# Optimization experiments

Measured on AMD Instinct MI355X. Metric: run time of the kernel, lower is better.

The kernel has to match this reference:

```python
import jax, jax.numpy as jnp
import numpy as np

K_HEADS, D_HEAD = 8, 8
D = K_HEADS * D_HEAD  # 64


def _fc(x, W, b=None, relu=False):
    # 1x1 Conv2D over (B,T,N,C) == per-position dense
    y = x @ W
    if b is not None:
        y = y + b
    return jax.nn.relu(y) if relu else y


def _split_heads(x):
    # (B,T,N,K*d) -> (K,B,T,N,d); matches torch.cat(torch.split(x, d, -1), 0)
    B, T, N, _ = x.shape
    return x.reshape(B, T, N, K_HEADS, D_HEAD).transpose(3, 0, 1, 2, 4)


def _merge_heads(x):
    # (K,B,T,N,d) -> (B,T,N,K*d); matches torch.cat(torch.split(x, B, 0), -1)
    K, B, T, N, d = x.shape
    return x.transpose(1, 2, 3, 0, 4).reshape(B, T, N, K * d)


def _forward(X, TLE, key_padding_mask, *P):
    (sa_Wq, sa_bq, sa_Wk, sa_bk, sa_Wv, sa_bv, sa_Wo1, sa_bo1, sa_Wo2, sa_bo2,
     ta_Wq, ta_bq, ta_Wk, ta_bk, ta_Wv, ta_bv, ta_Wo1, ta_bo1, ta_Wo2, ta_bo2,
     g_Wxs, g_Wxt, g_bxt, g_Wh1, g_bh1, g_Wh2, g_bh2) = P
    B, T, N, _ = X.shape
    scale = 1.0 / (D_HEAD ** 0.5)
    XE = jnp.concatenate([X, TLE], axis=-1)  # (B,T,N,3D)

    # ---- Spatial attention (over nodes) ----
    q = _split_heads(_fc(XE, sa_Wq, sa_bq, True))
    k = _split_heads(_fc(XE, sa_Wk, sa_bk, True))
    v = _split_heads(_fc(XE, sa_Wv, sa_bv, True))
    s = jnp.einsum('kbtnd,kbtmd->kbtnm', q, k) * scale  # (K,B,T,N,N)
    p = jax.nn.softmax(s, axis=-1)
    HS = _merge_heads(jnp.einsum('kbtnm,kbtmd->kbtnd', p, v))
    HS = _fc(_fc(HS, sa_Wo1, sa_bo1, True), sa_Wo2, sa_bo2)

    # ---- Temporal attention (over time, causal + key padding) ----
    q = _split_heads(_fc(XE, ta_Wq, ta_bq, True))
    k = _split_heads(_fc(XE, ta_Wk, ta_bk, True))
    v = _split_heads(_fc(XE, ta_Wv, ta_bv, True))
    s = jnp.einsum('kbind,kbjnd->kbnij', q, k) * scale  # (K,B,N,T,T)
    causal = jnp.tril(jnp.ones((T, T), dtype=bool))  # (T,T)
    valid_key = jnp.arange(T)[None, :] < key_padding_mask  # (B,T)
    m = causal[None, None, None] & valid_key[None, :, None, None, :]
    s = jnp.where(m, s, -jnp.inf)
    p = jax.nn.softmax(s, axis=-1)
    HT = _merge_heads(jnp.einsum('kbnij,kbjnd->kbind', p, v))
    HT = _fc(_fc(HT, ta_Wo1, ta_bo1, True), ta_Wo2, ta_bo2)

    # ---- Gated fusion + residual ----
    z = jax.nn.sigmoid(HS @ g_Wxs + HT @ g_Wxt + g_bxt)
    H = z * HS + (1.0 - z) * HT
    H = _fc(_fc(H, g_Wh1, g_bh1, True), g_Wh2, g_bh2)
    return X + H


_PARAM_SHAPES = []
for _pre in ('sa', 'ta'):
    _PARAM_SHAPES += [(_pre + '_Wq', (3 * D, D)), (_pre + '_bq', (D,)),
                      (_pre + '_Wk', (3 * D, D)), (_pre + '_bk', (D,)),
                      (_pre + '_Wv', (3 * D, D)), (_pre + '_bv', (D,)),
                      (_pre + '_Wo1', (D, D)), (_pre + '_bo1', (D,)),
                      (_pre + '_Wo2', (D, D)), (_pre + '_bo2', (D,))]
_PARAM_SHAPES += [('g_Wxs', (D, D)), ('g_Wxt', (D, D)), ('g_bxt', (D,)),
                  ('g_Wh1', (D, D)), ('g_bh1', (D,)),
                  ('g_Wh2', (D, D)), ('g_bh2', (D,))]


def setup_inputs() -> dict:
    key = jax.random.key(0)
    ks = jax.random.split(key, 3 + len(_PARAM_SHAPES))
    B, T, N = 16, 24, 128
    inp = {
        'X': jax.random.normal(ks[0], (B, T, N, D), dtype=jnp.float32),
        'TLE': jax.random.normal(ks[1], (B, T, N, 2 * D), dtype=jnp.float32),
        'key_padding_mask': jax.random.randint(ks[2], (B, 1), 1, T + 1),
    }
    for i, (nm, shp) in enumerate(_PARAM_SHAPES):
        inp[nm] = jax.random.normal(ks[3 + i], shp, dtype=jnp.float32) * 0.05
    return inp


def reference(X, TLE, key_padding_mask,
              sa_Wq, sa_bq, sa_Wk, sa_bk, sa_Wv, sa_bv, sa_Wo1, sa_bo1, sa_Wo2, sa_bo2,
              ta_Wq, ta_bq, ta_Wk, ta_bk, ta_Wv, ta_bv, ta_Wo1, ta_bo1, ta_Wo2, ta_bo2,
              g_Wxs, g_Wxt, g_bxt, g_Wh1, g_bh1, g_Wh2, g_bh2):
    return _forward(X, TLE, key_padding_mask,
                    sa_Wq, sa_bq, sa_Wk, sa_bk, sa_Wv, sa_bv, sa_Wo1, sa_bo1, sa_Wo2, sa_bo2,
                    ta_Wq, ta_bq, ta_Wk, ta_bk, ta_Wv, ta_bv, ta_Wo1, ta_bo1, ta_Wo2, ta_bo2,
                    g_Wxs, g_Wxt, g_bxt, g_Wh1, g_bh1, g_Wh2, g_bh2)
```

## Files before the change

kernel.cpp:

```cpp
#include <hip/hip_runtime.h>
#include <math.h>

#define BB 16
#define TT 24
#define NN 128
#define DD 64
#define PTOT (BB * TT * NN)
#define P64  (PTOT * 64)

typedef __attribute__((ext_vector_type(8))) short bf16x8;
typedef __attribute__((ext_vector_type(4))) float f32x4;
typedef __attribute__((ext_vector_type(16))) float f32x16;

__device__ __forceinline__ unsigned short f2bf(float f) {
    unsigned u = __builtin_bit_cast(unsigned, f);
    u = (u + 0x7fffu + ((u >> 16) & 1u)) >> 16;
    return (unsigned short)u;
}
__device__ __forceinline__ void unpack8(uint4 u, float* f) {
    f[0] = __builtin_bit_cast(float, u.x << 16);
    f[1] = __builtin_bit_cast(float, u.x & 0xFFFF0000u);
    f[2] = __builtin_bit_cast(float, u.y << 16);
    f[3] = __builtin_bit_cast(float, u.y & 0xFFFF0000u);
    f[4] = __builtin_bit_cast(float, u.z << 16);
    f[5] = __builtin_bit_cast(float, u.z & 0xFFFF0000u);
    f[6] = __builtin_bit_cast(float, u.w << 16);
    f[7] = __builtin_bit_cast(float, u.w & 0xFFFF0000u);
}
__device__ __forceinline__ uint4 pack8(const float* f) {
    uint4 o;
    o.x = (unsigned)f2bf(f[0]) | ((unsigned)f2bf(f[1]) << 16);
    o.y = (unsigned)f2bf(f[2]) | ((unsigned)f2bf(f[3]) << 16);
    o.z = (unsigned)f2bf(f[4]) | ((unsigned)f2bf(f[5]) << 16);
    o.w = (unsigned)f2bf(f[6]) | ((unsigned)f2bf(f[7]) << 16);
    return o;
}
__device__ __forceinline__ float fast_exp2(float x) {
#if __has_builtin(__builtin_amdgcn_exp2f)
    return __builtin_amdgcn_exp2f(x);
#else
    return exp2f(x);
#endif
}
__device__ __forceinline__ unsigned cvt_pk_bf16(float a, float b) {
    unsigned r;
    asm("v_cvt_pk_bf16_f32 %0, %1, %2" : "=v"(r) : "v"(a), "v"(b));
    return r;
}
__device__ __forceinline__ f32x16 zero16() {
    f32x16 z;
    #pragma unroll
    for (int i = 0; i < 16; ++i) z[i] = 0.f;
    return z;
}

__global__ __launch_bounds__(256) void wprep_all(
    const float* __restrict__ W0, const float* __restrict__ W1,
    const float* __restrict__ W2, const float* __restrict__ W3,
    const float* __restrict__ W4, const float* __restrict__ W5,
    const float* __restrict__ E0, const float* __restrict__ E1,
    const float* __restrict__ E2, const float* __restrict__ E3,
    const float* __restrict__ E4, const float* __restrict__ E5,
    const float* __restrict__ E6, const float* __restrict__ E7,
    unsigned short* __restrict__ Wt, unsigned short* __restrict__ Wt8)
{
    const int bid = blockIdx.x;
    if (bid < 288) {
        const float* Ws[6] = {W0, W1, W2, W3, W4, W5};
        const int e = bid * 256 + threadIdx.x;
        const int j = e / 12288;
        const int r = e % 12288;
        const int k = r / 64;
        const int n = r % 64;
        Wt[j * 12288 + n * 192 + k] = f2bf(Ws[j][k * 64 + n]);
    } else {
        const float* Es[8] = {E0, E1, E2, E3, E4, E5, E6, E7};
        const int e = (bid - 288) * 256 + threadIdx.x;
        const int mat = e >> 12;
        const int r = e & 4095;
        const int k = r >> 6;
        const int n = r & 63;
        Wt8[mat * 4096 + n * 64 + k] = f2bf(Es[mat][k * 64 + n]);
    }
}

__global__ __launch_bounds__(256, 2) void fused_sattn(
    const float* __restrict__ X, const float* __restrict__ TLE,
    const unsigned short* __restrict__ Wt,
    const float* __restrict__ b0, const float* __restrict__ b1,
    const float* __restrict__ b2, const float* __restrict__ b3,
    const float* __restrict__ b4, const float* __restrict__ b5,
    unsigned short* __restrict__ qt, unsigned short* __restrict__ kt,
    unsigned short* __restrict__ vt,
    unsigned short* __restrict__ HS)
{
    __shared__ __align__(16) unsigned short xe[2][16][200];
    __shared__ __align__(16) unsigned short qq[128 * 64];
    __shared__ __align__(16) unsigned short kk[128 * 64];
    __shared__ __align__(16) unsigned short vv[128 * 64];
    const int tid = threadIdx.x;
    const long p0 = (long)blockIdx.x * 128;
    const int w = tid >> 6, l = tid & 63, quad = l >> 4, l16 = l & 15;

    auto stage = [&](int mt, int buf) {
        #pragma unroll
        for (int i = 0; i < 3; ++i) {
            const int idx4 = tid + i * 256;
            const int m  = idx4 / 48;
            const int kq = idx4 % 48;
            const int k  = kq * 4;
            const long p = p0 + mt * 16 + m;
            float4 v;
            if (k < 64) v = *reinterpret_cast<const float4*>(X + p * 64 + k);
            else        v = *reinterpret_cast<const float4*>(TLE + p * 128 + (k - 64));
            ushort4 pk;
            pk.x = f2bf(v.x); pk.y = f2bf(v.y); pk.z = f2bf(v.z); pk.w = f2bf(v.w);
            *reinterpret_cast<ushort4*>(&xe[buf][m][k]) = pk;
        }
    };

    bf16x8 wf[6][6];
    #pragma unroll
    for (int mat = 0; mat < 6; ++mat)
        #pragma unroll
        for (int kc = 0; kc < 6; ++kc)
            wf[mat][kc] = *reinterpret_cast<const bf16x8*>(
                &Wt[mat * 12288 + (w * 16 + l16) * 192 + kc * 32 + quad * 8]);

    const float* bias_p[6] = {b0, b1, b2, b3, b4, b5};
    float4 bias[6];
    #pragma unroll
    for (int mat = 0; mat < 6; ++mat)
        bias[mat] = *reinterpret_cast<const float4*>(&bias_p[mat][w * 16 + quad * 4]);

    stage(0, 0);
    __syncthreads();

    const int chunkW = ((w * 2 + (quad >> 1)));
    const int chSub  = (quad & 1) * 4;
    const int chBase = w * 16 + quad * 4;
    const float cs = 0.35355339059327373f * 1.4426950408889634f;

    for (int mt = 0; mt < 8; ++mt) {
        if (mt < 7) stage(mt + 1, (mt + 1) & 1);

        bf16x8 A[6];
        #pragma unroll
        for (int kc = 0; kc < 6; ++kc)
            A[kc] = *reinterpret_cast<const bf16x8*>(
                &xe[mt & 1][l16][kc * 32 + quad * 8]);

        f32x4 acc[6];
        #pragma unroll
        for (int mat = 0; mat < 6; ++mat) acc[mat] = (f32x4){0.f, 0.f, 0.f, 0.f};
        #pragma unroll
        for (int kc = 0; kc < 6; ++kc)
            #pragma unroll
            for (int mat = 0; mat < 6; ++mat)
                acc[mat] = __builtin_amdgcn_mfma_f32_16x16x32_bf16(
                    wf[mat][kc], A[kc], acc[mat], 0, 0, 0);

        const int pos = mt * 16 + l16;
        const int sw  = pos * 64 + ((chunkW ^ (pos & 7)) << 3) + chSub;
        unsigned short* dstS[3] = {qq, kk, vv};
        #pragma unroll
        for (int mat = 0; mat < 3; ++mat) {
            const float sc = (mat == 0) ? cs : 1.0f;
            ushort4 pk;
            pk.x = f2bf(fmaxf(acc[mat][0] + bias[mat].x, 0.f) * sc);
            pk.y = f2bf(fmaxf(acc[mat][1] + bias[mat].y, 0.f) * sc);
            pk.z = f2bf(fmaxf(acc[mat][2] + bias[mat].z, 0.f) * sc);
            pk.w = f2bf(fmaxf(acc[mat][3] + bias[mat].w, 0.f) * sc);
            *reinterpret_cast<ushort4*>(&dstS[mat][sw]) = pk;
        }
        unsigned short* dstT[3] = {qt, kt, vt};
        const long gp = (p0 + pos) * 64 + chBase;
        #pragma unroll
        for (int m3 = 3; m3 < 6; ++m3) {
            ushort4 pk;
            pk.x = f2bf(fmaxf(acc[m3][0] + bias[m3].x, 0.f));
            pk.y = f2bf(fmaxf(acc[m3][1] + bias[m3].y, 0.f));
            pk.z = f2bf(fmaxf(acc[m3][2] + bias[m3].z, 0.f));
            pk.w = f2bf(fmaxf(acc[m3][3] + bias[m3].w, 0.f));
            *reinterpret_cast<ushort4*>(&dstT[m3 - 3][gp]) = pk;
        }
        if (mt < 7) {
            __builtin_amdgcn_sched_barrier(0);
            asm volatile("s_waitcnt lgkmcnt(0)" ::: "memory");
            __builtin_amdgcn_s_barrier();
            __builtin_amdgcn_sched_barrier(0);
        }
    }

    const int hi = l >> 5;
    const int ln = l & 31;
    bf16x8 zf = {};

    auto pvstep = [&](f32x16& st, const bf16x8& va0, const bf16x8& va1,
                      f32x16& oacc) {
        const unsigned P0 = cvt_pk_bf16(st[0],  st[1]);
        const unsigned P1 = cvt_pk_bf16(st[2],  st[3]);
        const unsigned P2 = cvt_pk_bf16(st[4],  st[5]);
        const unsigned P3 = cvt_pk_bf16(st[6],  st[7]);
        const unsigned P4 = cvt_pk_bf16(st[8],  st[9]);
        const unsigned P5 = cvt_pk_bf16(st[10], st[11]);
        const unsigned P6 = cvt_pk_bf16(st[12], st[13]);
        const unsigned P7 = cvt_pk_bf16(st[14], st[15]);
        const unsigned V0 = __shfl_xor(hi ? P0 : P2, 32);
        const unsigned V1 = __shfl_xor(hi ? P1 : P3, 32);
        const unsigned V2 = __shfl_xor(hi ? P4 : P6, 32);
        const unsigned V3 = __shfl_xor(hi ? P5 : P7, 32);
        uint4 fe, fo;
        fe.x = hi ? V0 : P0; fe.y = hi ? V1 : P1;
        fe.z = hi ? P2 : V0; fe.w = hi ? P3 : V1;
        fo.x = hi ? V2 : P4; fo.y = hi ? V3 : P5;
        fo.z = hi ? P6 : V2; fo.w = hi ? P7 : V3;
        oacc = __builtin_amdgcn_mfma_f32_32x32x16_bf16(
            va0, __builtin_bit_cast(bf16x8, fe), oacc, 0, 0, 0);
        oacc = __builtin_amdgcn_mfma_f32_32x32x16_bf16(
            va1, __builtin_bit_cast(bf16x8, fo), oacc, 0, 0, 0);
    };

    #pragma unroll
    for (int hh2 = 0; hh2 < 2; ++hh2) {
        const int h = w * 2 + hh2;
        const int swz = (h ^ (ln & 7)) << 3;

        bf16x8 kf0 = hi ? zf : *reinterpret_cast<const bf16x8*>(&kk[(0 * 32 + ln) * 64 + swz]);
        bf16x8 kf1 = hi ? zf : *reinterpret_cast<const bf16x8*>(&kk[(1 * 32 + ln) * 64 + swz]);
        bf16x8 kf2 = hi ? zf : *reinterpret_cast<const bf16x8*>(&kk[(2 * 32 + ln) * 64 + swz]);
        bf16x8 kf3 = hi ? zf : *reinterpret_cast<const bf16x8*>(&kk[(3 * 32 + ln) * 64 + swz]);

        bf16x8 vf[8];
        #pragma unroll
        for (int c = 0; c < 8; ++c) {
            bf16x8 f = zf;
            if (ln < 8) {
                #pragma unroll
                for (int j = 0; j < 8; ++j) {
                    const int m = c * 16 + hi * 8 + j;
                    f[j] = (short)vv[m * 64 + ((h ^ (m & 7)) << 3) + ln];
                }
            }
            vf[c] = f;
        }

        #pragma unroll
        for (int nt = 0; nt < 4; ++nt) {
            const int qrow = nt * 32 + ln;
            bf16x8 qf = hi ? zf : *reinterpret_cast<const bf16x8*>(&qq[qrow * 64 + swz]);

            f32x16 st0 = zero16(), st1 = zero16(), st2 = zero16(), st3 = zero16();
            st0 = __builtin_amdgcn_mfma_f32_32x32x16_bf16(kf0, qf, st0, 0, 0, 0);
            st1 = __builtin_amdgcn_mfma_f32_32x32x16_bf16(kf1, qf, st1, 0, 0, 0);
            st2 = __builtin_amdgcn_mfma_f32_32x32x16_bf16(kf2, qf, st2, 0, 0, 0);
            st3 = __builtin_amdgcn_mfma_f32_32x32x16_bf16(kf3, qf, st3, 0, 0, 0);

            float sum = 0.f;
            #pragma unroll
            for (int r = 0; r < 16; ++r) { st0[r] = fast_exp2(st0[r]); sum += st0[r]; }
            #pragma unroll
            for (int r = 0; r < 16; ++r) { st1[r] = fast_exp2(st1[r]); sum += st1[r]; }
            #pragma unroll
            for (int r = 0; r < 16; ++r) { st2[r] = fast_exp2(st2[r]); sum += st2[r]; }
            #pragma unroll
            for (int r = 0; r < 16; ++r) { st3[r] = fast_exp2(st3[r]); sum += st3[r]; }
            sum += __shfl_xor(sum, 32);

            f32x16 oacc = zero16();
            pvstep(st0, vf[0], vf[1], oacc);
            pvstep(st1, vf[2], vf[3], oacc);
            pvstep(st2, vf[4], vf[5], oacc);
            pvstep(st3, vf[6], vf[7], oacc);

            const float inv = 1.0f / sum;
            ushort4 pk;
            pk.x = f2bf(oacc[0] * inv);
            pk.y = f2bf(oacc[1] * inv);
            pk.z = f2bf(oacc[2] * inv);
            pk.w = f2bf(oacc[3] * inv);
            *reinterpret_cast<ushort4*>(&HS[(p0 + qrow) * 64 + h * 8 + hi * 4]) = pk;
        }
    }
}

__global__ __launch_bounds__(192) void tattn_kernel(
    const unsigned short* __restrict__ Q, const unsigned short* __restrict__ Kb,
    const unsigned short* __restrict__ V, const int* __restrict__ kpm,
    unsigned short* __restrict__ O)
{
    __shared__ float kk[8][TT][8];
    __shared__ float vv[8][TT][8];
    const int tid = threadIdx.x;
    const int n = blockIdx.x & (NN - 1);
    const int b = blockIdx.x >> 7;

    {
        const int hs = tid / TT;
        const int j  = tid % TT;
        const long g = (((long)(b * TT + j)) * NN + n) * 64 + hs * 8;
        uint4 ku = *reinterpret_cast<const uint4*>(&Kb[g]);
        uint4 vu = *reinterpret_cast<const uint4*>(&V[g]);
        float kf[8], vf[8];
        unpack8(ku, kf); unpack8(vu, vf);
        #pragma unroll
        for (int d = 0; d < 8; ++d) { kk[hs][j][d] = kf[d]; vv[hs][j][d] = vf[d]; }
    }

    const int h = tid / TT;
    const int i = tid % TT;
    const long qb = (((long)(b * TT + i)) * NN + n) * 64 + h * 8;
    float q[8];
    {
        uint4 qu = *reinterpret_cast<const uint4*>(&Q[qb]);
        unpack8(qu, q);
    }
    __syncthreads();

    const int kp = kpm[b];
    const float scale = 0.35355339059327373f;

    float s[TT];
    #pragma unroll
    for (int j = 0; j < TT; ++j) {
        float t = 0.0f;
        #pragma unroll
        for (int d = 0; d < 8; ++d) t = fmaf(q[d], kk[h][j][d], t);
        s[j] = (j <= i && j < kp) ? t * scale : -INFINITY;
    }
    float mx = -INFINITY;
    #pragma unroll
    for (int j = 0; j < TT; ++j) mx = fmaxf(mx, s[j]);

    float sum = 0.0f;
    float acc[8];
    #pragma unroll
    for (int d = 0; d < 8; ++d) acc[d] = 0.0f;
    #pragma unroll
    for (int j = 0; j < TT; ++j) {
        const float e = __expf(s[j] - mx);
        sum += e;
        #pragma unroll
        for (int d = 0; d < 8; ++d) acc[d] = fmaf(e, vv[h][j][d], acc[d]);
    }
    const float inv = 1.0f / sum;
    float o[8];
    #pragma unroll
    for (int d = 0; d < 8; ++d) o[d] = acc[d] * inv;
    *reinterpret_cast<uint4*>(&O[qb]) = pack8(o);
}

__global__ __launch_bounds__(256) void epi_kernel(
    const float* __restrict__ X,
    const unsigned short* __restrict__ HSb, const unsigned short* __restrict__ HTb,
    const unsigned short* __restrict__ Wt8,
    const float* __restrict__ sbo1, const float* __restrict__ sbo2,
    const float* __restrict__ tbo1, const float* __restrict__ tbo2,
    const float* __restrict__ bxt,
    const float* __restrict__ bh1, const float* __restrict__ bh2,
    float* __restrict__ out)
{
    constexpr int RS = 72;
    __shared__ __align__(16) unsigned short bufA[64][RS], bufB[64][RS], bufC[64][RS];
    const int tid = threadIdx.x;
    const long p0 = (long)blockIdx.x * 64;
    const int w = tid >> 6, l = tid & 63, quad = l >> 4, l16 = l & 15;
    const int chBase = w * 16 + quad * 4;

    #pragma unroll
    for (int i = 0; i < 4; ++i) {
        const int idx = tid + i * 256;
        const int m = idx >> 4;
        const int c = (idx & 15) * 4;
        *reinterpret_cast<ushort4*>(&bufA[m][c]) =
            *reinterpret_cast<const ushort4*>(&HSb[(p0 + m) * 64 + c]);
        *reinterpret_cast<ushort4*>(&bufC[m][c]) =
            *reinterpret_cast<const ushort4*>(&HTb[(p0 + m) * 64 + c]);
    }
    __syncthreads();

    auto gemm = [&](const unsigned short (*in)[RS], int mat,
                    const float* __restrict__ bias, f32x4* accO) {
        bf16x8 af[2];
        #pragma unroll
        for (int kc = 0; kc < 2; ++kc)
            af[kc] = *reinterpret_cast<const bf16x8*>(
                &Wt8[mat * 4096 + (w * 16 + l16) * 64 + kc * 32 + quad * 8]);
        const float4 b4 = *reinterpret_cast<const float4*>(&bias[chBase]);
        #pragma unroll
        for (int pt = 0; pt < 4; ++pt) {
            f32x4 acc = (f32x4){0.f, 0.f, 0.f, 0.f};
            #pragma unroll
            for (int kc = 0; kc < 2; ++kc) {
                bf16x8 bf = *reinterpret_cast<const bf16x8*>(
                    &in[pt * 16 + l16][kc * 32 + quad * 8]);
                acc = __builtin_amdgcn_mfma_f32_16x16x32_bf16(af[kc], bf, acc, 0, 0, 0);
            }
            acc[0] += b4.x; acc[1] += b4.y; acc[2] += b4.z; acc[3] += b4.w;
            accO[pt] = acc;
        }
    };

    auto writeBuf = [&](unsigned short (*dst)[RS], const f32x4* v, bool relu) {
        #pragma unroll
        for (int pt = 0; pt < 4; ++pt) {
            float a0 = v[pt][0], a1 = v[pt][1], a2 = v[pt][2], a3 = v[pt][3];
            if (relu) { a0 = fmaxf(a0, 0.f); a1 = fmaxf(a1, 0.f);
                        a2 = fmaxf(a2, 0.f); a3 = fmaxf(a3, 0.f); }
            ushort4 pk; pk.x = f2bf(a0); pk.y = f2bf(a1); pk.z = f2bf(a2); pk.w = f2bf(a3);
            *reinterpret_cast<ushort4*>(&dst[pt * 16 + l16][chBase]) = pk;
        }
    };

    f32x4 t[4], HSr[4], HTr[4];

    gemm(bufA, 0, sbo1, t);
    __syncthreads();
    writeBuf(bufB, t, true);
    __syncthreads();

    gemm(bufB, 1, sbo2, HSr);
    __syncthreads();
    writeBuf(bufA, HSr, false);
    __syncthreads();

    gemm(bufC, 2, tbo1, t);
    __syncthreads();
    writeBuf(bufB, t, true);
    __syncthreads();

    gemm(bufB, 3, tbo2, HTr);
    __syncthreads();
    writeBuf(bufC, HTr, false);
    __syncthreads();

    {
        bf16x8 afS[2], afT[2];
        #pragma unroll
        for (int kc = 0; kc < 2; ++kc) {
            afS[kc] = *reinterpret_cast<const bf16x8*>(
                &Wt8[4 * 4096 + (w * 16 + l16) * 64 + kc * 32 + quad * 8]);
            afT[kc] = *reinterpret_cast<const bf16x8*>(
                &Wt8[5 * 4096 + (w * 16 + l16) * 64 + kc * 32 + quad * 8]);
        }
        const float4 b4 = *reinterpret_cast<const float4*>(&bxt[chBase]);
        #pragma unroll
        for (int pt = 0; pt < 4; ++pt) {
            f32x4 acc = (f32x4){0.f, 0.f, 0.f, 0.f};
            #pragma unroll
            for (int kc = 0; kc < 2; ++kc) {
                bf16x8 hsf = *reinterpret_cast<const bf16x8*>(
                    &bufA[pt * 16 + l16][kc * 32 + quad * 8]);
                acc = __builtin_amdgcn_mfma_f32_16x16x32_bf16(afS[kc], hsf, acc, 0, 0, 0);
            }
            #pragma unroll
            for (int kc = 0; kc < 2; ++kc) {
                bf16x8 htf = *reinterpret_cast<const bf16x8*>(
                    &bufC[pt * 16 + l16][kc * 32 + quad * 8]);
                acc = __builtin_amdgcn_mfma_f32_16x16x32_bf16(afT[kc], htf, acc, 0, 0, 0);
            }
            const float zb[4] = {acc[0] + b4.x, acc[1] + b4.y, acc[2] + b4.z, acc[3] + b4.w};
            f32x4 h;
            #pragma unroll
            for (int r = 0; r < 4; ++r) {
                const float z = 1.0f / (1.0f + __expf(-zb[r]));
                h[r] = z * HSr[pt][r] + (1.0f - z) * HTr[pt][r];
            }
            t[pt] = h;
        }
    }
    __syncthreads();
    writeBuf(bufB, t, false);
    __syncthreads();

    gemm(bufB, 6, bh1, t);
    __syncthreads();
    writeBuf(bufA, t, true);
    __syncthreads();

    gemm(bufA, 7, bh2, t);
    #pragma unroll
    for (int pt = 0; pt < 4; ++pt) {
        const long pos = p0 + pt * 16 + l16;
        const float4 xv = *reinterpret_cast<const float4*>(&X[pos * 64 + chBase]);
        float4 o;
        o.x = t[pt][0] + xv.x; o.y = t[pt][1] + xv.y;
        o.z = t[pt][2] + xv.z; o.w = t[pt][3] + xv.w;
        *reinterpret_cast<float4*>(&out[pos * 64 + chBase]) = o;
    }
}

extern "C" void kernel_launch(void* const* d_in, const int* in_sizes, int n_in,
                              void* d_out, int out_size, void* d_ws, size_t ws_size,
                              hipStream_t stream) {
    const float* X   = (const float*)d_in[0];
    const float* TLE = (const float*)d_in[1];
    const int* kpm   = (const int*)d_in[2];

    const float* sa_Wq = (const float*)d_in[3];  const float* sa_bq = (const float*)d_in[4];
    const float* sa_Wk = (const float*)d_in[5];  const float* sa_bk = (const float*)d_in[6];
    const float* sa_Wv = (const float*)d_in[7];  const float* sa_bv = (const float*)d_in[8];
    const float* sa_Wo1 = (const float*)d_in[9];  const float* sa_bo1 = (const float*)d_in[10];
    const float* sa_Wo2 = (const float*)d_in[11]; const float* sa_bo2 = (const float*)d_in[12];
    const float* ta_Wq = (const float*)d_in[13]; const float* ta_bq = (const float*)d_in[14];
    const float* ta_Wk = (const float*)d_in[15]; const float* ta_bk = (const float*)d_in[16];
    const float* ta_Wv = (const float*)d_in[17]; const float* ta_bv = (const float*)d_in[18];
    const float* ta_Wo1 = (const float*)d_in[19]; const float* ta_bo1 = (const float*)d_in[20];
    const float* ta_Wo2 = (const float*)d_in[21]; const float* ta_bo2 = (const float*)d_in[22];
    const float* g_Wxs = (const float*)d_in[23];
    const float* g_Wxt = (const float*)d_in[24]; const float* g_bxt = (const float*)d_in[25];
    const float* g_Wh1 = (const float*)d_in[26]; const float* g_bh1 = (const float*)d_in[27];
    const float* g_Wh2 = (const float*)d_in[28]; const float* g_bh2 = (const float*)d_in[29];

    unsigned short* wsp = (unsigned short*)d_ws;
    unsigned short* qt  = wsp + 0L * P64;
    unsigned short* kt  = wsp + 1L * P64;
    unsigned short* vt  = wsp + 2L * P64;
    unsigned short* HSb = wsp + 3L * P64;
    unsigned short* HTb = wsp + 4L * P64;
    unsigned short* Wt  = wsp + 5L * P64;
    unsigned short* Wt8 = Wt + 6 * 12288;

    float* out = (float*)d_out;

    hipLaunchKernelGGL(wprep_all, dim3(416), dim3(256), 0, stream,
                       sa_Wq, sa_Wk, sa_Wv, ta_Wq, ta_Wk, ta_Wv,
                       sa_Wo1, sa_Wo2, ta_Wo1, ta_Wo2, g_Wxs, g_Wxt, g_Wh1, g_Wh2,
                       Wt, Wt8);

    hipLaunchKernelGGL(fused_sattn, dim3(BB * TT), dim3(256), 0, stream,
                       X, TLE, Wt,
                       sa_bq, sa_bk, sa_bv, ta_bq, ta_bk, ta_bv,
                       qt, kt, vt, HSb);

    hipLaunchKernelGGL(tattn_kernel, dim3(BB * NN), dim3(192), 0, stream,
                       qt, kt, vt, kpm, HTb);

    hipLaunchKernelGGL(epi_kernel, dim3(PTOT / 64), dim3(256), 0, stream,
                       X, HSb, HTb, Wt8,
                       sa_bo1, sa_bo2, ta_bo1, ta_bo2, g_bxt, g_bh1, g_bh2,
                       out);
}
```

Before: 82.12 us.

## Double fused spatial-attention block to 512 threads, splitting projections and heads across waves

The fused spatial attention kernel now launches 512 threads (8 waves) instead of 256. In the projection phase each wave handles 3 of the 6 weight matrices instead of all 6. In the attention phase each wave handles one head instead of two, and the score/softmax/PV loop is interleaved per key tile to reduce live registers. The intent is to halve per-thread register pressure and raise latency hiding and occupancy. In exchange, the last barrier iteration is no longer skipped, staging has a guarded idle half, and with 384 blocks the GPU may be underfilled at higher per-block width.

```diff
diff --git a/kernel.cpp b/kernel.cpp
--- a/kernel.cpp
+++ b/kernel.cpp
@@ -84,7 +84,7 @@
     }
 }
 
-__global__ __launch_bounds__(256, 2) void fused_sattn(
+__global__ __launch_bounds__(512, 4) void fused_sattn(
     const float* __restrict__ X, const float* __restrict__ TLE,
     const unsigned short* __restrict__ Wt,
     const float* __restrict__ b0, const float* __restrict__ b1,
@@ -101,44 +101,48 @@
     const int tid = threadIdx.x;
     const long p0 = (long)blockIdx.x * 128;
     const int w = tid >> 6, l = tid & 63, quad = l >> 4, l16 = l & 15;
+    const int nt = w >> 1;
+    const int mg = (w & 1) * 3;
 
     auto stage = [&](int mt, int buf) {
         #pragma unroll
-        for (int i = 0; i < 3; ++i) {
-            const int idx4 = tid + i * 256;
-            const int m  = idx4 / 48;
-            const int kq = idx4 % 48;
-            const int k  = kq * 4;
-            const long p = p0 + mt * 16 + m;
-            float4 v;
-            if (k < 64) v = *reinterpret_cast<const float4*>(X + p * 64 + k);
-            else        v = *reinterpret_cast<const float4*>(TLE + p * 128 + (k - 64));
-            ushort4 pk;
-            pk.x = f2bf(v.x); pk.y = f2bf(v.y); pk.z = f2bf(v.z); pk.w = f2bf(v.w);
-            *reinterpret_cast<ushort4*>(&xe[buf][m][k]) = pk;
+        for (int i = 0; i < 2; ++i) {
+            const int idx4 = tid + i * 512;
+            if (idx4 < 768) {
+                const int m  = idx4 / 48;
+                const int kq = idx4 % 48;
+                const int k  = kq * 4;
+                const long p = p0 + mt * 16 + m;
+                float4 v;
+                if (k < 64) v = *reinterpret_cast<const float4*>(X + p * 64 + k);
+                else        v = *reinterpret_cast<const float4*>(TLE + p * 128 + (k - 64));
+                ushort4 pk;
+                pk.x = f2bf(v.x); pk.y = f2bf(v.y); pk.z = f2bf(v.z); pk.w = f2bf(v.w);
+                *reinterpret_cast<ushort4*>(&xe[buf][m][k]) = pk;
+            }
         }
     };
 
-    bf16x8 wf[6][6];
-    #pragma unroll
-    for (int mat = 0; mat < 6; ++mat)
+    bf16x8 wf[3][6];
+    #pragma unroll
+    for (int mi = 0; mi < 3; ++mi)
         #pragma unroll
         for (int kc = 0; kc < 6; ++kc)
-            wf[mat][kc] = *reinterpret_cast<const bf16x8*>(
-                &Wt[mat * 12288 + (w * 16 + l16) * 192 + kc * 32 + quad * 8]);
+            wf[mi][kc] = *reinterpret_cast<const bf16x8*>(
+                &Wt[(mg + mi) * 12288 + (nt * 16 + l16) * 192 + kc * 32 + quad * 8]);
 
     const float* bias_p[6] = {b0, b1, b2, b3, b4, b5};
-    float4 bias[6];
-    #pragma unroll
-    for (int mat = 0; mat < 6; ++mat)
-        bias[mat] = *reinterpret_cast<const float4*>(&bias_p[mat][w * 16 + quad * 4]);
+    float4 bias[3];
+    #pragma unroll
+    for (int mi = 0; mi < 3; ++mi)
+        bias[mi] = *reinterpret_cast<const float4*>(&bias_p[mg + mi][nt * 16 + quad * 4]);
 
     stage(0, 0);
     __syncthreads();
 
-    const int chunkW = ((w * 2 + (quad >> 1)));
+    const int chBase = nt * 16 + quad * 4;
+    const int chunkW = nt * 2 + (quad >> 1);
     const int chSub  = (quad & 1) * 4;
-    const int chBase = w * 16 + quad * 4;
     const float cs = 0.35355339059327373f * 1.4426950408889634f;
 
     for (int mt = 0; mt < 8; ++mt) {
@@ -150,51 +154,54 @@
             A[kc] = *reinterpret_cast<const bf16x8*>(
                 &xe[mt & 1][l16][kc * 32 + quad * 8]);
 
-        f32x4 acc[6];
-        #pragma unroll
-        for (int mat = 0; mat < 6; ++mat) acc[mat] = (f32x4){0.f, 0.f, 0.f, 0.f};
+        f32x4 acc[3];
+        #pragma unroll
+        for (int mi = 0; mi < 3; ++mi) acc[mi] = (f32x4){0.f, 0.f, 0.f, 0.f};
         #pragma unroll
         for (int kc = 0; kc < 6; ++kc)
             #pragma unroll
-            for (int mat = 0; mat < 6; ++mat)
-                acc[mat] = __builtin_amdgcn_mfma_f32_16x16x32_bf16(
-                    wf[mat][kc], A[kc], acc[mat], 0, 0, 0);
+            for (int mi = 0; mi < 3; ++mi)
+                acc[mi] = __builtin_amdgcn_mfma_f32_16x16x32_bf16(
+                    wf[mi][kc], A[kc], acc[mi], 0, 0, 0);
 
         const int pos = mt * 16 + l16;
-        const int sw  = pos * 64 + ((chunkW ^ (pos & 7)) << 3) + chSub;
-        unsigned short* dstS[3] = {qq, kk, vv};
-        #pragma unroll
-        for (int mat = 0; mat < 3; ++mat) {
-            const float sc = (mat == 0) ? cs : 1.0f;
-            ushort4 pk;
-            pk.x = f2bf(fmaxf(acc[mat][0] + bias[mat].x, 0.f) * sc);
-            pk.y = f2bf(fmaxf(acc[mat][1] + bias[mat].y, 0.f) * sc);
-            pk.z = f2bf(fmaxf(acc[mat][2] + bias[mat].z, 0.f) * sc);
-            pk.w = f2bf(fmaxf(acc[mat][3] + bias[mat].w, 0.f) * sc);
-            *reinterpret_cast<ushort4*>(&dstS[mat][sw]) = pk;
-        }
-        unsigned short* dstT[3] = {qt, kt, vt};
-        const long gp = (p0 + pos) * 64 + chBase;
-        #pragma unroll
-        for (int m3 = 3; m3 < 6; ++m3) {
-            ushort4 pk;
-            pk.x = f2bf(fmaxf(acc[m3][0] + bias[m3].x, 0.f));
-            pk.y = f2bf(fmaxf(acc[m3][1] + bias[m3].y, 0.f));
-            pk.z = f2bf(fmaxf(acc[m3][2] + bias[m3].z, 0.f));
-            pk.w = f2bf(fmaxf(acc[m3][3] + bias[m3].w, 0.f));
-            *reinterpret_cast<ushort4*>(&dstT[m3 - 3][gp]) = pk;
-        }
-        if (mt < 7) {
-            __builtin_amdgcn_sched_barrier(0);
-            asm volatile("s_waitcnt lgkmcnt(0)" ::: "memory");
-            __builtin_amdgcn_s_barrier();
-            __builtin_amdgcn_sched_barrier(0);
-        }
-    }
-
+        if (mg == 0) {
+            const int sw = pos * 64 + ((chunkW ^ (pos & 7)) << 3) + chSub;
+            unsigned short* dstS[3] = {qq, kk, vv};
+            #pragma unroll
+            for (int mi = 0; mi < 3; ++mi) {
+                const float sc = (mi == 0) ? cs : 1.0f;
+                ushort4 pk;
+                pk.x = f2bf(fmaxf(acc[mi][0] + bias[mi].x, 0.f) * sc);
+                pk.y = f2bf(fmaxf(acc[mi][1] + bias[mi].y, 0.f) * sc);
+                pk.z = f2bf(fmaxf(acc[mi][2] + bias[mi].z, 0.f) * sc);
+                pk.w = f2bf(fmaxf(acc[mi][3] + bias[mi].w, 0.f) * sc);
+                *reinterpret_cast<ushort4*>(&dstS[mi][sw]) = pk;
+            }
+        } else {
+            unsigned short* dstT[3] = {qt, kt, vt};
+            const long gp = (p0 + pos) * 64 + chBase;
+            #pragma unroll
+            for (int mi = 0; mi < 3; ++mi) {
+                ushort4 pk;
+                pk.x = f2bf(fmaxf(acc[mi][0] + bias[mi].x, 0.f));
+                pk.y = f2bf(fmaxf(acc[mi][1] + bias[mi].y, 0.f));
+                pk.z = f2bf(fmaxf(acc[mi][2] + bias[mi].z, 0.f));
+                pk.w = f2bf(fmaxf(acc[mi][3] + bias[mi].w, 0.f));
+                *reinterpret_cast<ushort4*>(&dstT[mi][gp]) = pk;
+            }
+        }
+        __builtin_amdgcn_sched_barrier(0);
+        asm volatile("s_waitcnt lgkmcnt(0)" ::: "memory");
+        __builtin_amdgcn_s_barrier();
+        __builtin_amdgcn_sched_barrier(0);
+    }
+
+    const int h  = w;
     const int hi = l >> 5;
     const int ln = l & 31;
     bf16x8 zf = {};
+    const int swz = (h ^ (ln & 7)) << 3;
 
     auto pvstep = [&](f32x16& st, const bf16x8& va0, const bf16x8& va1,
                       f32x16& oacc) {
@@ -221,66 +228,49 @@
             va1, __builtin_bit_cast(bf16x8, fo), oacc, 0, 0, 0);
     };
 
-    #pragma unroll
-    for (int hh2 = 0; hh2 < 2; ++hh2) {
-        const int h = w * 2 + hh2;
-        const int swz = (h ^ (ln & 7)) << 3;
-
-        bf16x8 kf0 = hi ? zf : *reinterpret_cast<const bf16x8*>(&kk[(0 * 32 + ln) * 64 + swz]);
-        bf16x8 kf1 = hi ? zf : *reinterpret_cast<const bf16x8*>(&kk[(1 * 32 + ln) * 64 + swz]);
-        bf16x8 kf2 = hi ? zf : *reinterpret_cast<const bf16x8*>(&kk[(2 * 32 + ln) * 64 + swz]);
-        bf16x8 kf3 = hi ? zf : *reinterpret_cast<const bf16x8*>(&kk[(3 * 32 + ln) * 64 + swz]);
-
-        bf16x8 vf[8];
-        #pragma unroll
-        for (int c = 0; c < 8; ++c) {
-            bf16x8 f = zf;
-            if (ln < 8) {
-                #pragma unroll
-                for (int j = 0; j < 8; ++j) {
-                    const int m = c * 16 + hi * 8 + j;
-                    f[j] = (short)vv[m * 64 + ((h ^ (m & 7)) << 3) + ln];
-                }
-            }
-            vf[c] = f;
-        }
-
-        #pragma unroll
-        for (int nt = 0; nt < 4; ++nt) {
-            const int qrow = nt * 32 + ln;
-            bf16x8 qf = hi ? zf : *reinterpret_cast<const bf16x8*>(&qq[qrow * 64 + swz]);
-
-            f32x16 st0 = zero16(), st1 = zero16(), st2 = zero16(), st3 = zero16();
-            st0 = __builtin_amdgcn_mfma_f32_32x32x16_bf16(kf0, qf, st0, 0, 0, 0);
-            st1 = __builtin_amdgcn_mfma_f32_32x32x16_bf16(kf1, qf, st1, 0, 0, 0);
-            st2 = __builtin_amdgcn_mfma_f32_32x32x16_bf16(kf2, qf, st2, 0, 0, 0);
-            st3 = __builtin_amdgcn_mfma_f32_32x32x16_bf16(kf3, qf, st3, 0, 0, 0);
-
-            float sum = 0.f;
-            #pragma unroll
-            for (int r = 0; r < 16; ++r) { st0[r] = fast_exp2(st0[r]); sum += st0[r]; }
-            #pragma unroll
-            for (int r = 0; r < 16; ++r) { st1[r] = fast_exp2(st1[r]); sum += st1[r]; }
-            #pragma unroll
-            for (int r = 0; r < 16; ++r) { st2[r] = fast_exp2(st2[r]); sum += st2[r]; }
-            #pragma unroll
-            for (int r = 0; r < 16; ++r) { st3[r] = fast_exp2(st3[r]); sum += st3[r]; }
-            sum += __shfl_xor(sum, 32);
-
-            f32x16 oacc = zero16();
-            pvstep(st0, vf[0], vf[1], oacc);
-            pvstep(st1, vf[2], vf[3], oacc);
-            pvstep(st2, vf[4], vf[5], oacc);
-            pvstep(st3, vf[6], vf[7], oacc);
-
-            const float inv = 1.0f / sum;
-            ushort4 pk;
-            pk.x = f2bf(oacc[0] * inv);
-            pk.y = f2bf(oacc[1] * inv);
-            pk.z = f2bf(oacc[2] * inv);
-            pk.w = f2bf(oacc[3] * inv);
-            *reinterpret_cast<ushort4*>(&HS[(p0 + qrow) * 64 + h * 8 + hi * 4]) = pk;
-        }
+    bf16x8 kf[4];
+    #pragma unroll
+    for (int t = 0; t < 4; ++t)
+        kf[t] = hi ? zf : *reinterpret_cast<const bf16x8*>(&kk[(t * 32 + ln) * 64 + swz]);
+
+    bf16x8 vf[8];
+    #pragma unroll
+    for (int c = 0; c < 8; ++c) {
+        bf16x8 f = zf;
+        if (ln < 8) {
+            #pragma unroll
+            for (int j = 0; j < 8; ++j) {
+                const int m = c * 16 + hi * 8 + j;
+                f[j] = (short)vv[m * 64 + ((h ^ (m & 7)) << 3) + ln];
+            }
+        }
+        vf[c] = f;
+    }
+
+    #pragma unroll
+    for (int ntq = 0; ntq < 4; ++ntq) {
+        const int qrow = ntq * 32 + ln;
+        bf16x8 qf = hi ? zf : *reinterpret_cast<const bf16x8*>(&qq[qrow * 64 + swz]);
+
+        float sum = 0.f;
+        f32x16 oacc = zero16();
+        #pragma unroll
+        for (int t = 0; t < 4; ++t) {
+            f32x16 st = zero16();
+            st = __builtin_amdgcn_mfma_f32_32x32x16_bf16(kf[t], qf, st, 0, 0, 0);
+            #pragma unroll
+            for (int r = 0; r < 16; ++r) { st[r] = fast_exp2(st[r]); sum += st[r]; }
+            pvstep(st, vf[2 * t], vf[2 * t + 1], oacc);
+        }
+        sum += __shfl_xor(sum, 32);
+
+        const float inv = 1.0f / sum;
+        ushort4 pk;
+        pk.x = f2bf(oacc[0] * inv);
+        pk.y = f2bf(oacc[1] * inv);
+        pk.z = f2bf(oacc[2] * inv);
+        pk.w = f2bf(oacc[3] * inv);
+        *reinterpret_cast<ushort4*>(&HS[(p0 + qrow) * 64 + h * 8 + hi * 4]) = pk;
     }
 }
 
@@ -528,7 +518,7 @@
                        sa_Wo1, sa_Wo2, ta_Wo1, ta_Wo2, g_Wxs, g_Wxt, g_Wh1, g_Wh2,
                        Wt, Wt8);
 
-    hipLaunchKernelGGL(fused_sattn, dim3(BB * TT), dim3(256), 0, stream,
+    hipLaunchKernelGGL(fused_sattn, dim3(BB * TT), dim3(512), 0, stream,
                        X, TLE, Wt,
                        sa_bq, sa_bk, sa_bv, ta_bq, ta_bk, ta_bv,
                        qt, kt, vt, HSb);
```

After: 80.81 us. About the same (-1.6%).
